# Kernel tuning notes

Measured on AMD Instinct MI355X. Metric: run time of the kernel, lower is better.

Reference implementation:

```python
import jax, jax.numpy as jnp
import numpy as np

MERGE_COEFF = 0.5  # fixed beta-merge coefficient (init arg)


def setup_inputs() -> dict:
    key = jax.random.key(0)
    k1, k2, k3, k4 = jax.random.split(key, 4)
    N, M, H = 8192, 8192, 512
    s = 1.0 / np.sqrt(H)
    return {
        "features": jax.random.normal(k1, (N, H), dtype=jnp.float32),
        "memory_features": jax.random.normal(k2, (M, H), dtype=jnp.float32),
        "Wq": jax.random.normal(k3, (H, H), dtype=jnp.float32) * s,
        "bq": jnp.zeros((H,), dtype=jnp.float32),
        "Wk": jax.random.normal(k4, (H, H), dtype=jnp.float32) * s,
        "bk": jnp.zeros((H,), dtype=jnp.float32),
    }


def reference(features, memory_features, Wq, bq, Wk, bk):
    tau = 1.0
    # torch nn.Linear: y = x @ W.T + b
    q = features @ Wq.T + bq                 # [N, H]
    k = memory_features @ Wk.T + bk          # [M, H]
    attn = jax.nn.softmax((q @ k.T) / tau, axis=-1)  # [N, M]
    augment = attn @ memory_features          # [N, H]
    c = MERGE_COEFF
    return c * features + (1.0 - c) * augment
```

## Files before the change

kernel.cpp:

```cpp
#include <hip/hip_runtime.h>


typedef _Float16 half8 __attribute__((ext_vector_type(8)));
typedef _Float16 half4 __attribute__((ext_vector_type(4)));
typedef float floatx4 __attribute__((ext_vector_type(4)));

#define MFMA16(a, b, c) __builtin_amdgcn_mfma_f32_16x16x32_f16((a), (b), (c), 0, 0, 0)

static constexpr int H = 512;
static constexpr int NROWS = 8192;

__device__ __forceinline__ void dma16(half8* lds_dst, const void* g_src) {
    __builtin_amdgcn_global_load_lds(
        (const __attribute__((address_space(1))) unsigned int*)g_src,
        (__attribute__((address_space(3))) unsigned int*)lds_dst,
        16, 0, 0);
}

__global__ void castall_kernel(const float* __restrict__ F, const float* __restrict__ Mem,
                               const float* __restrict__ wq, const float* __restrict__ wk,
                               _Float16* __restrict__ f16, _Float16* __restrict__ m16,
                               _Float16* __restrict__ wq16, _Float16* __restrict__ wk16) {
    size_t i4 = (size_t)(blockIdx.x * 256 + threadIdx.x) * 4;
    const float* src; _Float16* dst; size_t off;
    if (i4 < 4194304ull)       { src = F;   dst = f16;  off = i4; }
    else if (i4 < 8388608ull)  { src = Mem; dst = m16;  off = i4 - 4194304ull; }
    else if (i4 < 8650752ull)  { src = wq;  dst = wq16; off = i4 - 8388608ull; }
    else                       { src = wk;  dst = wk16; off = i4 - 8650752ull; }
    float4 v = *(const float4*)&src[off];
    half4 h;
    h[0] = (_Float16)v.x; h[1] = (_Float16)v.y; h[2] = (_Float16)v.z; h[3] = (_Float16)v.w;
    *(half4*)&dst[off] = h;
}

__global__ void packv_kernel(const _Float16* __restrict__ m16, half8* __restrict__ vp) {
    const int kb = blockIdx.x;
    const int t  = threadIdx.x;
    const int c = t & 15, db = t >> 4;
    const _Float16* base = m16 + (size_t)kb * 32 * H + db * 16 + c;
#pragma unroll
    for (int g = 0; g < 4; ++g) {
        half8 v;
#pragma unroll
        for (int j = 0; j < 8; ++j) v[j] = base[(size_t)(g * 8 + j) * H];
        vp[(size_t)kb * 2048 + db * 64 + g * 16 + c] = v;
    }
}

__global__ __launch_bounds__(256, 4)
void proj_kernel(const _Float16* __restrict__ X16, const _Float16* __restrict__ W16,
                 const float* __restrict__ bias, _Float16* __restrict__ out) {
    const int lane = threadIdx.x & 63;
    const int wave = threadIdx.x >> 6;
    const int row0 = blockIdx.x * 128 + wave * 32;
    const int col0 = blockIdx.y * 64;
    const int lr = lane & 15, lq = lane >> 4;

    floatx4 acc[2][4];
#pragma unroll
    for (int rt = 0; rt < 2; ++rt)
#pragma unroll
        for (int nt = 0; nt < 4; ++nt) { acc[rt][nt][0] = 0.f; acc[rt][nt][1] = 0.f; acc[rt][nt][2] = 0.f; acc[rt][nt][3] = 0.f; }

    const half8* ar0 = (const half8*)(X16 + (size_t)(row0 + lr) * H) + lq;
    const half8* ar1 = (const half8*)(X16 + (size_t)(row0 + 16 + lr) * H) + lq;
    const half8* wbase = (const half8*)W16;

#pragma unroll
    for (int kk = 0; kk < 16; ++kk) {
        half8 a0 = ar0[kk * 4];
        half8 a1 = ar1[kk * 4];
#pragma unroll
        for (int nt = 0; nt < 4; ++nt) {
            half8 bf = wbase[(size_t)(col0 + nt * 16 + lr) * 64 + kk * 4 + lq];
            acc[0][nt] = MFMA16(a0, bf, acc[0][nt]);
            acc[1][nt] = MFMA16(a1, bf, acc[1][nt]);
        }
    }
#pragma unroll
    for (int rt = 0; rt < 2; ++rt)
#pragma unroll
        for (int nt = 0; nt < 4; ++nt) {
            int col = col0 + nt * 16 + lr;
            float b = bias[col];
#pragma unroll
            for (int r = 0; r < 4; ++r) {
                int row = row0 + rt * 16 + lq * 4 + r;
                out[(size_t)row * H + col] = (_Float16)(acc[rt][nt][r] + b);
            }
        }
}

__global__ __launch_bounds__(512, 2)
void flash_kernel(const _Float16* __restrict__ q16, const _Float16* __restrict__ k16,
                  const half8* __restrict__ vp, _Float16* __restrict__ opart,
                  float* __restrict__ mpart, float* __restrict__ lpart) {
    __shared__ half8 klds[2][2048];
    __shared__ half8 vlds[2][2048];
    __shared__ _Float16 plds[2][128 * 36];
    __shared__ float alds[2][128];
    __shared__ float llds[128];
    __shared__ int flagw[2][8];

    const int tid = threadIdx.x;
    const int lane = tid & 63;
    const int wave = tid >> 6;
    const int rbk = blockIdx.x >> 2;
    const int slice = blockIdx.x & 3;
    const int row0 = rbk * 128;
    const int lr = lane & 15, lq = lane >> 4;

    int koff[4];
#pragma unroll
    for (int i = 0; i < 4; ++i) {
        int d = tid + i * 512;
        int c = d >> 10, kk = (d >> 6) & 15, g = (d >> 4) & 3, cc = d & 15;
        koff[i] = c * 8192 + cc * 512 + kk * 32 + g * 8;
    }

    const half8* qrow = (const half8*)(q16 + (size_t)(row0 + wave * 16 + lr) * H);
    half8 qf[16];
#pragma unroll
    for (int kk = 0; kk < 16; ++kk) qf[kk] = qrow[kk * 4 + lq];

    floatx4 o[8][4];
#pragma unroll
    for (int rb = 0; rb < 8; ++rb)
#pragma unroll
        for (int f = 0; f < 4; ++f) { o[rb][f][0] = 0.f; o[rb][f][1] = 0.f; o[rb][f][2] = 0.f; o[rb][f][3] = 0.f; }
    float m[4], l[4];
#pragma unroll
    for (int r = 0; r < 4; ++r) { m[r] = -1e30f; l[r] = 0.f; }

    {
        const int kt0 = slice * 64;
        const _Float16* ksrc0 = k16 + (size_t)kt0 * 16384;
        const half8* vsrc0 = vp + (size_t)kt0 * 2048;
#pragma unroll
        for (int i = 0; i < 4; ++i) dma16(&klds[0][tid + i * 512], ksrc0 + koff[i]);
#pragma unroll
        for (int i = 0; i < 4; ++i) dma16(&vlds[0][tid + i * 512], &vsrc0[tid + i * 512]);
        const _Float16* ksrc1 = k16 + (size_t)(kt0 + 1) * 16384;
#pragma unroll
        for (int i = 0; i < 4; ++i) dma16(&klds[1][tid + i * 512], ksrc1 + koff[i]);
    }

    for (int tt = 0; tt < 64; ++tt) {
        const int b = tt & 1;

        asm volatile("s_waitcnt vmcnt(8) lgkmcnt(0)" ::: "memory");
        __builtin_amdgcn_s_barrier();

        if (tt > 0) {
            const int q1 = b ^ 1;
#pragma unroll
            for (int rb = 0; rb < 8; ++rb) {
                if (flagw[q1][rb]) {
                    float a0 = alds[q1][rb * 16 + lq * 4 + 0];
                    float a1 = alds[q1][rb * 16 + lq * 4 + 1];
                    float a2 = alds[q1][rb * 16 + lq * 4 + 2];
                    float a3 = alds[q1][rb * 16 + lq * 4 + 3];
#pragma unroll
                    for (int f = 0; f < 4; ++f) {
                        o[rb][f][0] *= a0; o[rb][f][1] *= a1;
                        o[rb][f][2] *= a2; o[rb][f][3] *= a3;
                    }
                }
            }
            __builtin_amdgcn_s_setprio(1);
            half8 vf[4];
#pragma unroll
            for (int f = 0; f < 4; ++f) vf[f] = vlds[q1][(wave * 4 + f) * 64 + lane];
#pragma unroll
            for (int rb = 0; rb < 8; ++rb) {
                half8 pfr = *(const half8*)&plds[q1][(rb * 16 + lr) * 36 + lq * 8];
#pragma unroll
                for (int f = 0; f < 4; ++f) o[rb][f] = MFMA16(pfr, vf[f], o[rb][f]);
            }
            __builtin_amdgcn_s_setprio(0);
        }

        __builtin_amdgcn_s_setprio(1);
        floatx4 s0 = {0.f, 0.f, 0.f, 0.f}, s1 = {0.f, 0.f, 0.f, 0.f};
#pragma unroll
        for (int kk = 0; kk < 16; ++kk) {
            s0 = MFMA16(qf[kk], klds[b][kk * 64 + lane], s0);
            s1 = MFMA16(qf[kk], klds[b][1024 + kk * 64 + lane], s1);
        }
        __builtin_amdgcn_s_setprio(0);

        float tm[4]; int trig = 0;
#pragma unroll
        for (int r = 0; r < 4; ++r) {
            tm[r] = fmaxf(s0[r], s1[r]);
            trig |= (tm[r] > m[r] + 10.f) ? 1 : 0;
        }
        const int trigany = __any(trig) ? 1 : 0;
        if (lane == 0) flagw[b][wave] = trigany;
        if (trigany) {
            float al[4];
#pragma unroll
            for (int r = 0; r < 4; ++r) {
                float mx = tm[r];
                mx = fmaxf(mx, __shfl_xor(mx, 1));
                mx = fmaxf(mx, __shfl_xor(mx, 2));
                mx = fmaxf(mx, __shfl_xor(mx, 4));
                mx = fmaxf(mx, __shfl_xor(mx, 8));
                float mn = (mx > m[r] + 10.f) ? mx : m[r];
                al[r] = __expf(m[r] - mn);
                m[r] = mn;
                l[r] *= al[r];
            }
            if (lr == 0) {
#pragma unroll
                for (int r = 0; r < 4; ++r) alds[b][wave * 16 + lq * 4 + r] = al[r];
            }
        }

#pragma unroll
        for (int r = 0; r < 4; ++r) {
            float p0 = __expf(s0[r] - m[r]);
            float p1 = __expf(s1[r] - m[r]);
            l[r] += p0 + p1;
            plds[b][(wave * 16 + lq * 4 + r) * 36 + lr]      = (_Float16)p0;
            plds[b][(wave * 16 + lq * 4 + r) * 36 + 16 + lr] = (_Float16)p1;
        }

        asm volatile("s_waitcnt lgkmcnt(0)" ::: "memory");
        __builtin_amdgcn_s_barrier();

        {
            int vt = tt + 1; if (vt > 63) vt = 63;
            int kt2 = tt + 2; if (kt2 > 63) kt2 = 63;
            const half8* vsrc = vp + (size_t)(slice * 64 + vt) * 2048;
#pragma unroll
            for (int i = 0; i < 4; ++i) dma16(&vlds[(tt + 1) & 1][tid + i * 512], &vsrc[tid + i * 512]);
            const _Float16* ksrc = k16 + (size_t)(slice * 64 + kt2) * 16384;
#pragma unroll
            for (int i = 0; i < 4; ++i) dma16(&klds[b][tid + i * 512], ksrc + koff[i]);
        }
    }

    asm volatile("s_waitcnt lgkmcnt(0)" ::: "memory");
    {
#pragma unroll
        for (int rb = 0; rb < 8; ++rb) {
            if (flagw[1][rb]) {
                float a0 = alds[1][rb * 16 + lq * 4 + 0];
                float a1 = alds[1][rb * 16 + lq * 4 + 1];
                float a2 = alds[1][rb * 16 + lq * 4 + 2];
                float a3 = alds[1][rb * 16 + lq * 4 + 3];
#pragma unroll
                for (int f = 0; f < 4; ++f) {
                    o[rb][f][0] *= a0; o[rb][f][1] *= a1;
                    o[rb][f][2] *= a2; o[rb][f][3] *= a3;
                }
            }
        }
        __builtin_amdgcn_s_setprio(1);
        half8 vf[4];
#pragma unroll
        for (int f = 0; f < 4; ++f) vf[f] = vlds[1][(wave * 4 + f) * 64 + lane];
#pragma unroll
        for (int rb = 0; rb < 8; ++rb) {
            half8 pfr = *(const half8*)&plds[1][(rb * 16 + lr) * 36 + lq * 8];
#pragma unroll
            for (int f = 0; f < 4; ++f) o[rb][f] = MFMA16(pfr, vf[f], o[rb][f]);
        }
        __builtin_amdgcn_s_setprio(0);
    }

#pragma unroll
    for (int r = 0; r < 4; ++r) {
        float lv = l[r];
        lv += __shfl_xor(lv, 1); lv += __shfl_xor(lv, 2);
        lv += __shfl_xor(lv, 4); lv += __shfl_xor(lv, 8);
        l[r] = lv;
    }
    if (lr == 0) {
#pragma unroll
        for (int r = 0; r < 4; ++r) {
            int row = wave * 16 + lq * 4 + r;
            llds[row] = l[r];
            mpart[slice * NROWS + row0 + row] = m[r];
            lpart[slice * NROWS + row0 + row] = l[r];
        }
    }
    __syncthreads();

    _Float16* ob = opart + (size_t)slice * NROWS * H;
#pragma unroll
    for (int rb = 0; rb < 8; ++rb) {
#pragma unroll
        for (int rr = 0; rr < 4; ++rr) {
            float linv = 1.0f / llds[rb * 16 + lq * 4 + rr];
            size_t row = row0 + rb * 16 + lq * 4 + rr;
#pragma unroll
            for (int f = 0; f < 4; ++f)
                ob[row * H + wave * 64 + f * 16 + lr] = (_Float16)(o[rb][f][rr] * linv);
        }
    }
}

__global__ void merge_kernel(const _Float16* __restrict__ opart, const float* __restrict__ mpart,
                             const float* __restrict__ lpart, const float* __restrict__ F,
                             float* __restrict__ out) {
    int gid = blockIdx.x * 256 + threadIdx.x;
    size_t idx4 = (size_t)gid * 4;
    int row = (int)(idx4 >> 9);
    float m0 = mpart[row], m1 = mpart[NROWS + row], m2 = mpart[2 * NROWS + row], m3 = mpart[3 * NROWS + row];
    float ms = fmaxf(fmaxf(m0, m1), fmaxf(m2, m3));
    float w0 = __expf(m0 - ms) * lpart[row];
    float w1 = __expf(m1 - ms) * lpart[NROWS + row];
    float w2 = __expf(m2 - ms) * lpart[2 * NROWS + row];
    float w3 = __expf(m3 - ms) * lpart[3 * NROWS + row];
    float rdenom = 1.0f / (w0 + w1 + w2 + w3);
    size_t stride = (size_t)NROWS * H;
    half4 o0 = *(const half4*)&opart[idx4];
    half4 o1 = *(const half4*)&opart[stride + idx4];
    half4 o2 = *(const half4*)&opart[2 * stride + idx4];
    half4 o3 = *(const half4*)&opart[3 * stride + idx4];
    float4 Fv = *(const float4*)&F[idx4];
    float4 res;
    res.x = 0.5f * Fv.x + 0.5f * ((w0 * (float)o0[0] + w1 * (float)o1[0] + w2 * (float)o2[0] + w3 * (float)o3[0]) * rdenom);
    res.y = 0.5f * Fv.y + 0.5f * ((w0 * (float)o0[1] + w1 * (float)o1[1] + w2 * (float)o2[1] + w3 * (float)o3[1]) * rdenom);
    res.z = 0.5f * Fv.z + 0.5f * ((w0 * (float)o0[2] + w1 * (float)o1[2] + w2 * (float)o2[2] + w3 * (float)o3[2]) * rdenom);
    res.w = 0.5f * Fv.w + 0.5f * ((w0 * (float)o0[3] + w1 * (float)o1[3] + w2 * (float)o2[3] + w3 * (float)o3[3]) * rdenom);
    *(float4*)&out[idx4] = res;
}

extern "C" void kernel_launch(void* const* d_in, const int* in_sizes, int n_in,
                              void* d_out, int out_size, void* d_ws, size_t ws_size,
                              hipStream_t stream) {
    const float* F   = (const float*)d_in[0];
    const float* Mem = (const float*)d_in[1];
    const float* Wq  = (const float*)d_in[2];
    const float* bq  = (const float*)d_in[3];
    const float* Wk  = (const float*)d_in[4];
    const float* bk  = (const float*)d_in[5];
    float* out = (float*)d_out;

    char* ws = (char*)d_ws;
    _Float16* q16   = (_Float16*)(ws);
    _Float16* k16   = (_Float16*)(ws + (8ull << 20));
    half8*    vp    = (half8*)(ws + (16ull << 20));
    _Float16* opart = (_Float16*)(ws + (24ull << 20));
    _Float16* f16F  = (_Float16*)(ws + (24ull << 20));
    _Float16* m16   = (_Float16*)(ws + (32ull << 20));
    float*    mpart = (float*)(ws + (56ull << 20));
    float*    lpart = (float*)(ws + (56ull << 20) + (128ull << 10));
    _Float16* wq16  = (_Float16*)(ws + (57ull << 20));
    _Float16* wk16  = (_Float16*)(ws + (57ull << 20) + (512ull << 10));

    castall_kernel<<<8704, 256, 0, stream>>>(F, Mem, Wq, Wk, f16F, m16, wq16, wk16);
    packv_kernel<<<256, 512, 0, stream>>>(m16, vp);
    proj_kernel<<<dim3(64, 8), 256, 0, stream>>>(f16F, wq16, bq, q16);
    proj_kernel<<<dim3(64, 8), 256, 0, stream>>>(m16, wk16, bk, k16);
    flash_kernel<<<256, 512, 0, stream>>>(q16, k16, vp, opart, mpart, lpart);
    merge_kernel<<<4096, 256, 0, stream>>>(opart, mpart, lpart, F, out);
}
```

Before: 339.8 us.

## Halve flash block rows and load V fragments directly into registers

The flash kernel now uses 64-row blocks with 4 waves instead of 128 rows with 8, and launches twice as many blocks. Each wave covers 128 output columns. V fragments are loaded from global memory straight into registers, double-buffered across a two-tile unrolled loop, so the V staging buffers in LDS go away. This cuts LDS use and the V DMA traffic, and the larger grid of smaller blocks should fill the device better. The cost is that each V tile is read from global memory per block with no LDS sharing, K tiles are loaded twice as often overall, and register pressure rises.

```diff
diff --git a/kernel.cpp b/kernel.cpp
--- a/kernel.cpp
+++ b/kernel.cpp
@@ -91,29 +91,129 @@
         }
 }
 
-__global__ __launch_bounds__(512, 2)
+template<int B>
+__device__ __forceinline__ void flash_tile(
+    int tt, int tid, int lane, int wave, int lr, int lq, int slice,
+    const half8* __restrict__ vp, const _Float16* __restrict__ k16,
+    const int (&koff)[8],
+    half8 (&klds)[2][2048], _Float16 (&plds)[2][64 * 36],
+    float (&alds)[2][64], int (&flagw)[2][4],
+    const half8 (&qf)[16], half8 (&vfP)[8], half8 (&vfC)[8],
+    floatx4 (&o)[4][8], float (&m)[4], float (&l)[4]) {
+
+    asm volatile("s_waitcnt vmcnt(8) lgkmcnt(0)" ::: "memory");
+    __builtin_amdgcn_s_barrier();
+
+    {
+        const half8* vsrc = vp + (size_t)(slice * 64 + tt) * 2048 + wave * 512 + lane;
+#pragma unroll
+        for (int f = 0; f < 8; ++f) vfC[f] = vsrc[f * 64];
+    }
+
+    if (tt > 0) {
+#pragma unroll
+        for (int rb = 0; rb < 4; ++rb) {
+            if (flagw[B ^ 1][rb]) {
+                float a0 = alds[B ^ 1][rb * 16 + lq * 4 + 0];
+                float a1 = alds[B ^ 1][rb * 16 + lq * 4 + 1];
+                float a2 = alds[B ^ 1][rb * 16 + lq * 4 + 2];
+                float a3 = alds[B ^ 1][rb * 16 + lq * 4 + 3];
+#pragma unroll
+                for (int f = 0; f < 8; ++f) {
+                    o[rb][f][0] *= a0; o[rb][f][1] *= a1;
+                    o[rb][f][2] *= a2; o[rb][f][3] *= a3;
+                }
+            }
+        }
+        __builtin_amdgcn_s_setprio(1);
+#pragma unroll
+        for (int rb = 0; rb < 4; ++rb) {
+            half8 pfr = *(const half8*)&plds[B ^ 1][(rb * 16 + lr) * 36 + lq * 8];
+#pragma unroll
+            for (int f = 0; f < 8; ++f) o[rb][f] = MFMA16(pfr, vfP[f], o[rb][f]);
+        }
+        __builtin_amdgcn_s_setprio(0);
+    }
+
+    __builtin_amdgcn_s_setprio(1);
+    floatx4 s0 = {0.f, 0.f, 0.f, 0.f}, s1 = {0.f, 0.f, 0.f, 0.f};
+#pragma unroll
+    for (int kk = 0; kk < 16; ++kk) {
+        s0 = MFMA16(qf[kk], klds[B][kk * 64 + lane], s0);
+        s1 = MFMA16(qf[kk], klds[B][1024 + kk * 64 + lane], s1);
+    }
+    __builtin_amdgcn_s_setprio(0);
+
+    float tm[4]; int trig = 0;
+#pragma unroll
+    for (int r = 0; r < 4; ++r) {
+        tm[r] = fmaxf(s0[r], s1[r]);
+        trig |= (tm[r] > m[r] + 10.f) ? 1 : 0;
+    }
+    const int trigany = __any(trig) ? 1 : 0;
+    if (lane == 0) flagw[B][wave] = trigany;
+    if (trigany) {
+        float al[4];
+#pragma unroll
+        for (int r = 0; r < 4; ++r) {
+            float mx = tm[r];
+            mx = fmaxf(mx, __shfl_xor(mx, 1));
+            mx = fmaxf(mx, __shfl_xor(mx, 2));
+            mx = fmaxf(mx, __shfl_xor(mx, 4));
+            mx = fmaxf(mx, __shfl_xor(mx, 8));
+            float mn = (mx > m[r] + 10.f) ? mx : m[r];
+            al[r] = __expf(m[r] - mn);
+            m[r] = mn;
+            l[r] *= al[r];
+        }
+        if (lr == 0) {
+#pragma unroll
+            for (int r = 0; r < 4; ++r) alds[B][wave * 16 + lq * 4 + r] = al[r];
+        }
+    }
+
+#pragma unroll
+    for (int r = 0; r < 4; ++r) {
+        float p0 = __expf(s0[r] - m[r]);
+        float p1 = __expf(s1[r] - m[r]);
+        l[r] += p0 + p1;
+        plds[B][(wave * 16 + lq * 4 + r) * 36 + lr]      = (_Float16)p0;
+        plds[B][(wave * 16 + lq * 4 + r) * 36 + 16 + lr] = (_Float16)p1;
+    }
+
+    asm volatile("s_waitcnt lgkmcnt(0)" ::: "memory");
+    __builtin_amdgcn_s_barrier();
+
+    {
+        int kt2 = tt + 2; if (kt2 > 63) kt2 = 63;
+        const _Float16* ksrc = k16 + (size_t)(slice * 64 + kt2) * 16384;
+#pragma unroll
+        for (int i = 0; i < 8; ++i) dma16(&klds[B][tid + i * 256], ksrc + koff[i]);
+    }
+}
+
+__global__ __launch_bounds__(256, 2)
 void flash_kernel(const _Float16* __restrict__ q16, const _Float16* __restrict__ k16,
                   const half8* __restrict__ vp, _Float16* __restrict__ opart,
                   float* __restrict__ mpart, float* __restrict__ lpart) {
     __shared__ half8 klds[2][2048];
-    __shared__ half8 vlds[2][2048];
-    __shared__ _Float16 plds[2][128 * 36];
-    __shared__ float alds[2][128];
-    __shared__ float llds[128];
-    __shared__ int flagw[2][8];
+    __shared__ _Float16 plds[2][64 * 36];
+    __shared__ float alds[2][64];
+    __shared__ float llds[64];
+    __shared__ int flagw[2][4];
 
     const int tid = threadIdx.x;
     const int lane = tid & 63;
     const int wave = tid >> 6;
     const int rbk = blockIdx.x >> 2;
     const int slice = blockIdx.x & 3;
-    const int row0 = rbk * 128;
+    const int row0 = rbk * 64;
     const int lr = lane & 15, lq = lane >> 4;
 
-    int koff[4];
-#pragma unroll
-    for (int i = 0; i < 4; ++i) {
-        int d = tid + i * 512;
+    int koff[8];
+#pragma unroll
+    for (int i = 0; i < 8; ++i) {
+        int d = tid + i * 256;
         int c = d >> 10, kk = (d >> 6) & 15, g = (d >> 4) & 3, cc = d & 15;
         koff[i] = c * 8192 + cc * 512 + kk * 32 + g * 8;
     }
@@ -123,149 +223,56 @@
 #pragma unroll
     for (int kk = 0; kk < 16; ++kk) qf[kk] = qrow[kk * 4 + lq];
 
-    floatx4 o[8][4];
-#pragma unroll
-    for (int rb = 0; rb < 8; ++rb)
-#pragma unroll
-        for (int f = 0; f < 4; ++f) { o[rb][f][0] = 0.f; o[rb][f][1] = 0.f; o[rb][f][2] = 0.f; o[rb][f][3] = 0.f; }
+    floatx4 o[4][8];
+#pragma unroll
+    for (int rb = 0; rb < 4; ++rb)
+#pragma unroll
+        for (int f = 0; f < 8; ++f) { o[rb][f][0] = 0.f; o[rb][f][1] = 0.f; o[rb][f][2] = 0.f; o[rb][f][3] = 0.f; }
     float m[4], l[4];
 #pragma unroll
     for (int r = 0; r < 4; ++r) { m[r] = -1e30f; l[r] = 0.f; }
+    half8 vf0[8], vf1[8];
 
     {
         const int kt0 = slice * 64;
         const _Float16* ksrc0 = k16 + (size_t)kt0 * 16384;
-        const half8* vsrc0 = vp + (size_t)kt0 * 2048;
-#pragma unroll
-        for (int i = 0; i < 4; ++i) dma16(&klds[0][tid + i * 512], ksrc0 + koff[i]);
-#pragma unroll
-        for (int i = 0; i < 4; ++i) dma16(&vlds[0][tid + i * 512], &vsrc0[tid + i * 512]);
+#pragma unroll
+        for (int i = 0; i < 8; ++i) dma16(&klds[0][tid + i * 256], ksrc0 + koff[i]);
         const _Float16* ksrc1 = k16 + (size_t)(kt0 + 1) * 16384;
 #pragma unroll
-        for (int i = 0; i < 4; ++i) dma16(&klds[1][tid + i * 512], ksrc1 + koff[i]);
-    }
-
-    for (int tt = 0; tt < 64; ++tt) {
-        const int b = tt & 1;
-
-        asm volatile("s_waitcnt vmcnt(8) lgkmcnt(0)" ::: "memory");
-        __builtin_amdgcn_s_barrier();
-
-        if (tt > 0) {
-            const int q1 = b ^ 1;
-#pragma unroll
-            for (int rb = 0; rb < 8; ++rb) {
-                if (flagw[q1][rb]) {
-                    float a0 = alds[q1][rb * 16 + lq * 4 + 0];
-                    float a1 = alds[q1][rb * 16 + lq * 4 + 1];
-                    float a2 = alds[q1][rb * 16 + lq * 4 + 2];
-                    float a3 = alds[q1][rb * 16 + lq * 4 + 3];
-#pragma unroll
-                    for (int f = 0; f < 4; ++f) {
-                        o[rb][f][0] *= a0; o[rb][f][1] *= a1;
-                        o[rb][f][2] *= a2; o[rb][f][3] *= a3;
-                    }
-                }
-            }
-            __builtin_amdgcn_s_setprio(1);
-            half8 vf[4];
-#pragma unroll
-            for (int f = 0; f < 4; ++f) vf[f] = vlds[q1][(wave * 4 + f) * 64 + lane];
-#pragma unroll
-            for (int rb = 0; rb < 8; ++rb) {
-                half8 pfr = *(const half8*)&plds[q1][(rb * 16 + lr) * 36 + lq * 8];
-#pragma unroll
-                for (int f = 0; f < 4; ++f) o[rb][f] = MFMA16(pfr, vf[f], o[rb][f]);
-            }
-            __builtin_amdgcn_s_setprio(0);
-        }
-
-        __builtin_amdgcn_s_setprio(1);
-        floatx4 s0 = {0.f, 0.f, 0.f, 0.f}, s1 = {0.f, 0.f, 0.f, 0.f};
-#pragma unroll
-        for (int kk = 0; kk < 16; ++kk) {
-            s0 = MFMA16(qf[kk], klds[b][kk * 64 + lane], s0);
-            s1 = MFMA16(qf[kk], klds[b][1024 + kk * 64 + lane], s1);
-        }
-        __builtin_amdgcn_s_setprio(0);
-
-        float tm[4]; int trig = 0;
-#pragma unroll
-        for (int r = 0; r < 4; ++r) {
-            tm[r] = fmaxf(s0[r], s1[r]);
-            trig |= (tm[r] > m[r] + 10.f) ? 1 : 0;
-        }
-        const int trigany = __any(trig) ? 1 : 0;
-        if (lane == 0) flagw[b][wave] = trigany;
-        if (trigany) {
-            float al[4];
-#pragma unroll
-            for (int r = 0; r < 4; ++r) {
-                float mx = tm[r];
-                mx = fmaxf(mx, __shfl_xor(mx, 1));
-                mx = fmaxf(mx, __shfl_xor(mx, 2));
-                mx = fmaxf(mx, __shfl_xor(mx, 4));
-                mx = fmaxf(mx, __shfl_xor(mx, 8));
-                float mn = (mx > m[r] + 10.f) ? mx : m[r];
-                al[r] = __expf(m[r] - mn);
-                m[r] = mn;
-                l[r] *= al[r];
-            }
-            if (lr == 0) {
-#pragma unroll
-                for (int r = 0; r < 4; ++r) alds[b][wave * 16 + lq * 4 + r] = al[r];
-            }
-        }
-
-#pragma unroll
-        for (int r = 0; r < 4; ++r) {
-            float p0 = __expf(s0[r] - m[r]);
-            float p1 = __expf(s1[r] - m[r]);
-            l[r] += p0 + p1;
-            plds[b][(wave * 16 + lq * 4 + r) * 36 + lr]      = (_Float16)p0;
-            plds[b][(wave * 16 + lq * 4 + r) * 36 + 16 + lr] = (_Float16)p1;
-        }
-
-        asm volatile("s_waitcnt lgkmcnt(0)" ::: "memory");
-        __builtin_amdgcn_s_barrier();
-
-        {
-            int vt = tt + 1; if (vt > 63) vt = 63;
-            int kt2 = tt + 2; if (kt2 > 63) kt2 = 63;
-            const half8* vsrc = vp + (size_t)(slice * 64 + vt) * 2048;
-#pragma unroll
-            for (int i = 0; i < 4; ++i) dma16(&vlds[(tt + 1) & 1][tid + i * 512], &vsrc[tid + i * 512]);
-            const _Float16* ksrc = k16 + (size_t)(slice * 64 + kt2) * 16384;
-#pragma unroll
-            for (int i = 0; i < 4; ++i) dma16(&klds[b][tid + i * 512], ksrc + koff[i]);
-        }
-    }
-
-    asm volatile("s_waitcnt lgkmcnt(0)" ::: "memory");
+        for (int i = 0; i < 8; ++i) dma16(&klds[1][tid + i * 256], ksrc1 + koff[i]);
+    }
+
+    for (int tt2 = 0; tt2 < 64; tt2 += 2) {
+        flash_tile<0>(tt2,     tid, lane, wave, lr, lq, slice, vp, k16, koff,
+                      klds, plds, alds, flagw, qf, vf1, vf0, o, m, l);
+        flash_tile<1>(tt2 + 1, tid, lane, wave, lr, lq, slice, vp, k16, koff,
+                      klds, plds, alds, flagw, qf, vf0, vf1, o, m, l);
+    }
+
+    asm volatile("s_waitcnt vmcnt(0) lgkmcnt(0)" ::: "memory");
+    __builtin_amdgcn_s_barrier();
     {
 #pragma unroll
-        for (int rb = 0; rb < 8; ++rb) {
+        for (int rb = 0; rb < 4; ++rb) {
             if (flagw[1][rb]) {
                 float a0 = alds[1][rb * 16 + lq * 4 + 0];
                 float a1 = alds[1][rb * 16 + lq * 4 + 1];
                 float a2 = alds[1][rb * 16 + lq * 4 + 2];
                 float a3 = alds[1][rb * 16 + lq * 4 + 3];
 #pragma unroll
-                for (int f = 0; f < 4; ++f) {
+                for (int f = 0; f < 8; ++f) {
                     o[rb][f][0] *= a0; o[rb][f][1] *= a1;
                     o[rb][f][2] *= a2; o[rb][f][3] *= a3;
                 }
             }
         }
         __builtin_amdgcn_s_setprio(1);
-        half8 vf[4];
-#pragma unroll
-        for (int f = 0; f < 4; ++f) vf[f] = vlds[1][(wave * 4 + f) * 64 + lane];
-#pragma unroll
-        for (int rb = 0; rb < 8; ++rb) {
+#pragma unroll
+        for (int rb = 0; rb < 4; ++rb) {
             half8 pfr = *(const half8*)&plds[1][(rb * 16 + lr) * 36 + lq * 8];
 #pragma unroll
-            for (int f = 0; f < 4; ++f) o[rb][f] = MFMA16(pfr, vf[f], o[rb][f]);
+            for (int f = 0; f < 8; ++f) o[rb][f] = MFMA16(pfr, vf1[f], o[rb][f]);
         }
         __builtin_amdgcn_s_setprio(0);
     }
@@ -290,14 +297,14 @@
 
     _Float16* ob = opart + (size_t)slice * NROWS * H;
 #pragma unroll
-    for (int rb = 0; rb < 8; ++rb) {
+    for (int rb = 0; rb < 4; ++rb) {
 #pragma unroll
         for (int rr = 0; rr < 4; ++rr) {
             float linv = 1.0f / llds[rb * 16 + lq * 4 + rr];
             size_t row = row0 + rb * 16 + lq * 4 + rr;
 #pragma unroll
-            for (int f = 0; f < 4; ++f)
-                ob[row * H + wave * 64 + f * 16 + lr] = (_Float16)(o[rb][f][rr] * linv);
+            for (int f = 0; f < 8; ++f)
+                ob[row * H + wave * 128 + f * 16 + lr] = (_Float16)(o[rb][f][rr] * linv);
         }
     }
 }
@@ -356,6 +363,6 @@
     packv_kernel<<<256, 512, 0, stream>>>(m16, vp);
     proj_kernel<<<dim3(64, 8), 256, 0, stream>>>(f16F, wq16, bq, q16);
     proj_kernel<<<dim3(64, 8), 256, 0, stream>>>(m16, wk16, bk, k16);
-    flash_kernel<<<256, 512, 0, stream>>>(q16, k16, vp, opart, mpart, lpart);
+    flash_kernel<<<512, 256, 0, stream>>>(q16, k16, vp, opart, mpart, lpart);
     merge_kernel<<<4096, 256, 0, stream>>>(opart, mpart, lpart, F, out);
 }
```

Result: slower. 712.6 us (+109.7%).
